# Performance work log

Measured on AMD Instinct MI355X. Metric: run time of the kernel, lower is better.

The kernel has to match this reference:

```python
import jax, jax.numpy as jnp
import numpy as np

N = 100000          # num nodes
E = 1_600_000       # num edges (avg degree 16)
IN = 512
OUT = 64
HOPS = 4


def setup_inputs() -> dict:
    key = jax.random.key(0)
    k1, k2, k3 = jax.random.split(key, 3)
    x = jax.random.normal(k1, (N, IN), dtype=jnp.float32)
    W = jax.random.normal(k2, (OUT, IN), dtype=jnp.float32) * 0.02
    b = jnp.zeros((OUT,), dtype=jnp.float32)
    edge_index = jax.random.randint(k3, (2, E), 0, N, dtype=jnp.int32)
    return {"x": x, "W": W, "b": b, "edge_index": edge_index}


def reference(x, W, b, edge_index):
    # 1) linear projection first (low-memory SGC variant)
    h = x @ W.T + b                      # [N, OUT]
    n = h.shape[0]

    # 2) gcn_norm: add self loops, symmetric D^{-1/2} A D^{-1/2}
    row, col = edge_index[0], edge_index[1]
    loop = jnp.arange(n, dtype=row.dtype)
    row = jnp.concatenate([row, loop])   # [E+N]
    col = jnp.concatenate([col, loop])
    ew = jnp.ones(row.shape[0], dtype=h.dtype)
    deg = jax.ops.segment_sum(ew, col, num_segments=n)          # in-degree incl. self loop
    dinv = jnp.where(deg > 0, jax.lax.rsqrt(deg), 0.0)
    w = dinv[row] * ew * dinv[col]       # normalized edge weights [E+N]

    # 3) hops x SpMM: adj_t built with (row=col, col=row) => out[col] += w * h[row]
    for _ in range(HOPS):
        h = jax.ops.segment_sum(w[:, None] * h[row], col, num_segments=n)
    return h
```

## Files before the change

kernel.cpp:

```cpp
#include <hip/hip_runtime.h>
#include <stdint.h>

#define IN_DIM 512
#define OUT_DIM 64

typedef short bf16x8 __attribute__((ext_vector_type(8)));
typedef float f32x4 __attribute__((ext_vector_type(4)));
typedef _Float16 half4v __attribute__((ext_vector_type(4)));

__device__ inline unsigned short f2bf(float f) {
    unsigned int u = __float_as_uint(f);
    return (unsigned short)((u + 0x7FFFu + ((u >> 16) & 1u)) >> 16);
}
__device__ inline float bf2f(unsigned short s) {
    return __uint_as_float(((unsigned int)s) << 16);
}

__global__ void zero_deg_kernel(int* __restrict__ deg, int N) {
    int i = blockIdx.x * blockDim.x + threadIdx.x;
    if (i < N) deg[i] = 0;
}

__global__ __launch_bounds__(256) void hist_part_kernel(const int* __restrict__ col,
                                                        int* __restrict__ deg, int E, int N) {
    int part = blockIdx.x & 7;
    int lo = (int)((long)part * N / 8);
    int hi = (int)((long)(part + 1) * N / 8);
    int stride = (gridDim.x >> 3) * blockDim.x;
    int i = (blockIdx.x >> 3) * blockDim.x + threadIdx.x;
    for (; i < E; i += stride) {
        int c = col[i];
        if (c >= lo && c < hi) atomicAdd(&deg[c], 1);
    }
}

__global__ void dinv_kernel(const int* __restrict__ deg, float* __restrict__ dinv,
                            float* __restrict__ d2, int N) {
    int i = blockIdx.x * blockDim.x + threadIdx.x;
    if (i < N) {
        float d = (float)deg[i] + 1.0f;
        dinv[i] = 1.0f / sqrtf(d);
        d2[i] = 1.0f / d;
    }
}

__global__ void pack_w_kernel(const float* __restrict__ W,
                              unsigned short* __restrict__ Bhi,
                              unsigned short* __restrict__ Blo) {
    int tid = blockIdx.x * blockDim.x + threadIdx.x;
    if (tid >= 4096) return;
    int L = tid & 63;
    int ct = tid >> 6;
    int t = ct & 15, c = ct >> 4;
    int o = c * 16 + (L & 15);
    int k0 = t * 32 + (L >> 4) * 8;
    const float* src = W + (size_t)o * IN_DIM + k0;
    #pragma unroll
    for (int j = 0; j < 8; ++j) {
        float w = src[j];
        unsigned short h = f2bf(w);
        Bhi[(size_t)tid * 8 + j] = h;
        Blo[(size_t)tid * 8 + j] = f2bf(w - bf2f(h));
    }
}

__global__ __launch_bounds__(1024) void scan_local_kernel(const int* __restrict__ deg,
                                                          int* __restrict__ rowptr,
                                                          int* __restrict__ bsum, int N) {
    __shared__ int sm[16];
    int tid = threadIdx.x, lane = tid & 63, wid = tid >> 6;
    int i = blockIdx.x * 4096 + tid * 4;
    int4 v = make_int4(0, 0, 0, 0);
    if (i + 3 < N) {
        v = *(const int4*)(deg + i);
    } else {
        if (i < N) v.x = deg[i];
        if (i + 1 < N) v.y = deg[i + 1];
        if (i + 2 < N) v.z = deg[i + 2];
        if (i + 3 < N) v.w = deg[i + 3];
    }
    int s1 = v.x, s2 = s1 + v.y, s3 = s2 + v.z, s4 = s3 + v.w;
    int incl = s4;
    #pragma unroll
    for (int d = 1; d < 64; d <<= 1) {
        int t = __shfl_up(incl, d, 64);
        if (lane >= d) incl += t;
    }
    if (lane == 63) sm[wid] = incl;
    __syncthreads();
    if (tid == 0) {
        int run = 0;
        #pragma unroll
        for (int w2 = 0; w2 < 16; ++w2) { int t = sm[w2]; sm[w2] = run; run += t; }
        bsum[blockIdx.x] = run;
    }
    __syncthreads();
    int tbase = incl - s4 + sm[wid];
    if (i + 3 < N) {
        *(int4*)(rowptr + i) = make_int4(tbase, tbase + s1, tbase + s2, tbase + s3);
    } else {
        if (i < N)     rowptr[i]     = tbase;
        if (i + 1 < N) rowptr[i + 1] = tbase + s1;
        if (i + 2 < N) rowptr[i + 2] = tbase + s2;
        if (i + 3 < N) rowptr[i + 3] = tbase + s3;
    }
}

__global__ __launch_bounds__(1024) void scan_add_kernel(int* __restrict__ rowptr,
                                                        int* __restrict__ cursor,
                                                        const int* __restrict__ bsum,
                                                        int N, int nb) {
    __shared__ int soff;
    if (threadIdx.x == 0) {
        int off = 0;
        for (int j = 0; j < (int)blockIdx.x; ++j) off += bsum[j];
        soff = off;
        if ((int)blockIdx.x == nb - 1) {
            int tot = off;
            for (int j = blockIdx.x; j < nb; ++j) tot += bsum[j];
            rowptr[N] = tot;
        }
    }
    __syncthreads();
    int off = soff;
    int i = blockIdx.x * 4096 + threadIdx.x * 4;
    if (i + 3 < N) {
        int4 r = *(int4*)(rowptr + i);
        r.x += off; r.y += off; r.z += off; r.w += off;
        *(int4*)(rowptr + i) = r;
        *(int4*)(cursor + i) = r;
    } else {
        for (int j = 0; j < 4; ++j)
            if (i + j < N) { int r = rowptr[i + j] + off; rowptr[i + j] = r; cursor[i + j] = r; }
    }
}

__global__ __launch_bounds__(256) void fill_part_kernel(const int* __restrict__ row,
                                                        const int* __restrict__ col,
                                                        int* __restrict__ cursor,
                                                        int* __restrict__ csr, int E, int N) {
    int part = blockIdx.x & 7;
    int lo = (int)((long)part * N / 8);
    int hi = (int)((long)(part + 1) * N / 8);
    int stride = (gridDim.x >> 3) * blockDim.x;
    int i = (blockIdx.x >> 3) * blockDim.x + threadIdx.x;
    for (; i < E; i += stride) {
        int c = col[i];
        if (c >= lo && c < hi) {
            int pos = atomicAdd(&cursor[c], 1);
            csr[pos] = row[i];
        }
    }
}

__global__ __launch_bounds__(256) void mfma_gemm_kernel(const float* __restrict__ x,
                                                        const unsigned short* __restrict__ Bhi,
                                                        const unsigned short* __restrict__ Blo,
                                                        const float* __restrict__ bias,
                                                        const float* __restrict__ dinv,
                                                        _Float16* __restrict__ h, int N) {
    int lane = threadIdx.x & 63;
    int wid  = __builtin_amdgcn_readfirstlane(threadIdx.x >> 6);
    int quad = lane >> 4, r16 = lane & 15;
    long rowBase = ((long)blockIdx.x * 4 + wid) * 32;
    if (rowBase >= N) return;
    bool full = (rowBase + 32 <= N);

    f32x4 acc[2][4];
    #pragma unroll
    for (int rt = 0; rt < 2; ++rt)
        #pragma unroll
        for (int c = 0; c < 4; ++c) acc[rt][c] = (f32x4){0.f, 0.f, 0.f, 0.f};

    int row0 = (int)rowBase + r16;
    int row1 = (int)rowBase + 16 + r16;
    int row0c = full ? row0 : (row0 < N ? row0 : N - 1);
    int row1c = full ? row1 : (row1 < N ? row1 : N - 1);
    const float* a0p = x + (size_t)row0c * IN_DIM + quad * 8;
    const float* a1p = x + (size_t)row1c * IN_DIM + quad * 8;

    for (int t = 0; t < 16; ++t) {
        bf16x8 bh[4], bl[4];
        #pragma unroll
        for (int c = 0; c < 4; ++c) {
            size_t off = ((size_t)(c * 16 + t) * 64 + lane) * 8;
            union { int4 i; bf16x8 b; } uh, ul;
            uh.i = *(const int4*)(Bhi + off);
            ul.i = *(const int4*)(Blo + off);
            bh[c] = uh.b; bl[c] = ul.b;
        }
        bf16x8 ah[2], al[2];
        #pragma unroll
        for (int rt = 0; rt < 2; ++rt) {
            const float* p = (rt ? a1p : a0p) + t * 32;
            float4 f0 = *(const float4*)p;
            float4 f1 = *(const float4*)(p + 4);
            float v[8] = {f0.x, f0.y, f0.z, f0.w, f1.x, f1.y, f1.z, f1.w};
            #pragma unroll
            for (int j = 0; j < 8; ++j) {
                unsigned short hi = f2bf(v[j]);
                ah[rt][j] = (short)hi;
                al[rt][j] = (short)f2bf(v[j] - bf2f(hi));
            }
        }
        #pragma unroll
        for (int rt = 0; rt < 2; ++rt)
            #pragma unroll
            for (int c = 0; c < 4; ++c) {
                acc[rt][c] = __builtin_amdgcn_mfma_f32_16x16x32_bf16(ah[rt], bh[c], acc[rt][c], 0, 0, 0);
                acc[rt][c] = __builtin_amdgcn_mfma_f32_16x16x32_bf16(ah[rt], bl[c], acc[rt][c], 0, 0, 0);
                acc[rt][c] = __builtin_amdgcn_mfma_f32_16x16x32_bf16(al[rt], bh[c], acc[rt][c], 0, 0, 0);
            }
    }

    float bb[4];
    #pragma unroll
    for (int c = 0; c < 4; ++c) bb[c] = bias[c * 16 + r16];
    #pragma unroll
    for (int rt = 0; rt < 2; ++rt)
        #pragma unroll
        for (int rr = 0; rr < 4; ++rr) {
            int row = (int)rowBase + rt * 16 + quad * 4 + rr;
            if (row < N) {
                float dv = dinv[row];
                #pragma unroll
                for (int c = 0; c < 4; ++c)
                    h[(size_t)row * OUT_DIM + c * 16 + r16] =
                        (_Float16)(dv * (acc[rt][c][rr] + bb[c]));
            }
        }
}

#define HOP_K 8

__global__ __launch_bounds__(256) void hop_kernel(const _Float16* __restrict__ src,
                                                  _Float16* __restrict__ dst_h,
                                                  float* __restrict__ dst_f,
                                                  const int* __restrict__ csr,
                                                  const int* __restrict__ rowptr,
                                                  const float* __restrict__ scale,
                                                  int N, int finalOut) {
    int lane = threadIdx.x & 63;
    int wid  = __builtin_amdgcn_readfirstlane(threadIdx.x >> 6);
    int g    = lane >> 4;
    int l16  = lane & 15;
    int w  = blockIdx.x * 4 + wid;
    int n0 = w * HOP_K;
    if (n0 >= N) return;
    int nK = (N - n0 < HOP_K) ? (N - n0) : HOP_K;

    int rpv = 0;
    if (lane <= nK) rpv = rowptr[n0 + lane];

    for (int j = 0; j < nK; ++j) {
        int n = n0 + j;
        int s = __shfl(rpv, j, 64);
        int e = __shfl(rpv, j + 1, 64);

        float a0 = 0.f, a1 = 0.f, a2 = 0.f, a3 = 0.f;
        int i = s;
        for (; i + 16 <= e; i += 16) {
            int base = i + 4 * g;
            int i0 = csr[base], i1 = csr[base + 1], i2 = csr[base + 2], i3 = csr[base + 3];
            half4v v0 = *(const half4v*)(src + (size_t)i0 * OUT_DIM + l16 * 4);
            half4v v1 = *(const half4v*)(src + (size_t)i1 * OUT_DIM + l16 * 4);
            half4v v2 = *(const half4v*)(src + (size_t)i2 * OUT_DIM + l16 * 4);
            half4v v3 = *(const half4v*)(src + (size_t)i3 * OUT_DIM + l16 * 4);
            a0 += ((float)v0[0] + (float)v1[0]) + ((float)v2[0] + (float)v3[0]);
            a1 += ((float)v0[1] + (float)v1[1]) + ((float)v2[1] + (float)v3[1]);
            a2 += ((float)v0[2] + (float)v1[2]) + ((float)v2[2] + (float)v3[2]);
            a3 += ((float)v0[3] + (float)v1[3]) + ((float)v2[3] + (float)v3[3]);
        }
        for (; i + 4 <= e; i += 4) {
            int i0 = csr[i + g];
            half4v v = *(const half4v*)(src + (size_t)i0 * OUT_DIM + l16 * 4);
            a0 += (float)v[0]; a1 += (float)v[1]; a2 += (float)v[2]; a3 += (float)v[3];
        }
        if (i + g < e) {
            int i0 = csr[i + g];
            half4v v = *(const half4v*)(src + (size_t)i0 * OUT_DIM + l16 * 4);
            a0 += (float)v[0]; a1 += (float)v[1]; a2 += (float)v[2]; a3 += (float)v[3];
        }
        #pragma unroll
        for (int d = 16; d < 64; d <<= 1) {
            a0 += __shfl_xor(a0, d, 64);
            a1 += __shfl_xor(a1, d, 64);
            a2 += __shfl_xor(a2, d, 64);
            a3 += __shfl_xor(a3, d, 64);
        }
        if (lane < 16) {
            half4v s4 = *(const half4v*)(src + (size_t)n * OUT_DIM + l16 * 4);
            float sc = scale[n];
            float r0 = (a0 + (float)s4[0]) * sc;
            float r1 = (a1 + (float)s4[1]) * sc;
            float r2 = (a2 + (float)s4[2]) * sc;
            float r3 = (a3 + (float)s4[3]) * sc;
            if (finalOut) {
                f32x4 r = (f32x4){r0, r1, r2, r3};
                *(f32x4*)(dst_f + (size_t)n * OUT_DIM + l16 * 4) = r;
            } else {
                half4v o;
                o[0] = (_Float16)r0; o[1] = (_Float16)r1;
                o[2] = (_Float16)r2; o[3] = (_Float16)r3;
                *(half4v*)(dst_h + (size_t)n * OUT_DIM + l16 * 4) = o;
            }
        }
    }
}

extern "C" void kernel_launch(void* const* d_in, const int* in_sizes, int n_in,
                              void* d_out, int out_size, void* d_ws, size_t ws_size,
                              hipStream_t stream) {
    const float* x  = (const float*)d_in[0];
    const float* W  = (const float*)d_in[1];
    const float* b  = (const float*)d_in[2];
    const int*   ei = (const int*)d_in[3];
    int N = in_sizes[0] / IN_DIM;
    int E = in_sizes[3] / 2;
    const int* row = ei;
    const int* col = ei + E;
    float* out = (float*)d_out;

    float* dinv   = (float*)d_ws;
    float* d2     = dinv + N;
    int*   deg    = (int*)(d2 + N);
    int*   rowptr = deg + N;
    int*   cursor = rowptr + (N + 4);
    int*   bsum   = cursor + N;
    unsigned short* Bhi = (unsigned short*)(bsum + 32);
    unsigned short* Blo = Bhi + 32768;

    _Float16* gout = (_Float16*)d_out;
    float* xspace = (float*)d_in[0];
    _Float16* gx   = (_Float16*)xspace;
    int* csr = (int*)((char*)xspace + (size_t)N * OUT_DIM * sizeof(_Float16));

    dim3 blk(256);
    int gN = (N + 255) / 256;
    int gPart = 8 * 784;
    int nbScan = (N + 4095) / 4096;

    zero_deg_kernel<<<gN, blk, 0, stream>>>(deg, N);
    hist_part_kernel<<<gPart, blk, 0, stream>>>(col, deg, E, N);
    dinv_kernel<<<gN, blk, 0, stream>>>(deg, dinv, d2, N);

    pack_w_kernel<<<16, blk, 0, stream>>>(W, Bhi, Blo);

    mfma_gemm_kernel<<<(N + 127) / 128, blk, 0, stream>>>(x, Bhi, Blo, b, dinv, gout, N);

    scan_local_kernel<<<nbScan, 1024, 0, stream>>>(deg, rowptr, bsum, N);
    scan_add_kernel<<<nbScan, 1024, 0, stream>>>(rowptr, cursor, bsum, N, nbScan);
    fill_part_kernel<<<gPart, blk, 0, stream>>>(row, col, cursor, csr, E, N);

    int chunks = (N + HOP_K - 1) / HOP_K;
    int gH = (chunks + 3) / 4;
    hop_kernel<<<gH, blk, 0, stream>>>(gout, gx,   nullptr, csr, rowptr, d2,   N, 0);
    hop_kernel<<<gH, blk, 0, stream>>>(gx,   gout, nullptr, csr, rowptr, d2,   N, 0);
    hop_kernel<<<gH, blk, 0, stream>>>(gout, gx,   nullptr, csr, rowptr, d2,   N, 0);
    hop_kernel<<<gH, blk, 0, stream>>>(gx, nullptr, out,    csr, rowptr, dinv, N, 1);
}
```

Measured before the change: 666.6 us.

## Split hop features into 16-wide column slabs with XCD-aware block mapping

The GEMM now writes the projected features as four column-major slabs of 16 halves per node. Each hop kernel block handles one slab, so every gathered row is 32 bytes and the working set per slab is about 3.2MB, small enough to stay in cache. The block index is mapped so that the same slab lands on consistent XCDs, and a persistent grid of 2048 blocks is used. CSR indices and outputs use nontemporal loads and stores. In exchange, CSR indices and rowptr are read four times, once per slab, and lanes with clamped indices still issue redundant loads.

```diff
diff --git a/kernel.cpp b/kernel.cpp
--- a/kernel.cpp
+++ b/kernel.cpp
@@ -225,13 +225,14 @@
                 float dv = dinv[row];
                 #pragma unroll
                 for (int c = 0; c < 4; ++c)
-                    h[(size_t)row * OUT_DIM + c * 16 + r16] =
+                    h[((size_t)c * N + row) * 16 + r16] =
                         (_Float16)(dv * (acc[rt][c][rr] + bb[c]));
             }
         }
 }
 
 #define HOP_K 8
+#define HOP_BLOCKS 2048
 
 __global__ __launch_bounds__(256) void hop_kernel(const _Float16* __restrict__ src,
                                                   _Float16* __restrict__ dst_h,
@@ -242,67 +243,84 @@
                                                   int N, int finalOut) {
     int lane = threadIdx.x & 63;
     int wid  = __builtin_amdgcn_readfirstlane(threadIdx.x >> 6);
-    int g    = lane >> 4;
-    int l16  = lane & 15;
-    int w  = blockIdx.x * 4 + wid;
-    int n0 = w * HOP_K;
-    if (n0 >= N) return;
-    int nK = (N - n0 < HOP_K) ? (N - n0) : HOP_K;
-
-    int rpv = 0;
-    if (lane <= nK) rpv = rowptr[n0 + lane];
-
-    for (int j = 0; j < nK; ++j) {
-        int n = n0 + j;
-        int s = __shfl(rpv, j, 64);
-        int e = __shfl(rpv, j + 1, 64);
-
-        float a0 = 0.f, a1 = 0.f, a2 = 0.f, a3 = 0.f;
-        int i = s;
-        for (; i + 16 <= e; i += 16) {
-            int base = i + 4 * g;
-            int i0 = csr[base], i1 = csr[base + 1], i2 = csr[base + 2], i3 = csr[base + 3];
-            half4v v0 = *(const half4v*)(src + (size_t)i0 * OUT_DIM + l16 * 4);
-            half4v v1 = *(const half4v*)(src + (size_t)i1 * OUT_DIM + l16 * 4);
-            half4v v2 = *(const half4v*)(src + (size_t)i2 * OUT_DIM + l16 * 4);
-            half4v v3 = *(const half4v*)(src + (size_t)i3 * OUT_DIM + l16 * 4);
-            a0 += ((float)v0[0] + (float)v1[0]) + ((float)v2[0] + (float)v3[0]);
-            a1 += ((float)v0[1] + (float)v1[1]) + ((float)v2[1] + (float)v3[1]);
-            a2 += ((float)v0[2] + (float)v1[2]) + ((float)v2[2] + (float)v3[2]);
-            a3 += ((float)v0[3] + (float)v1[3]) + ((float)v2[3] + (float)v3[3]);
-        }
-        for (; i + 4 <= e; i += 4) {
-            int i0 = csr[i + g];
-            half4v v = *(const half4v*)(src + (size_t)i0 * OUT_DIM + l16 * 4);
-            a0 += (float)v[0]; a1 += (float)v[1]; a2 += (float)v[2]; a3 += (float)v[3];
-        }
-        if (i + g < e) {
-            int i0 = csr[i + g];
-            half4v v = *(const half4v*)(src + (size_t)i0 * OUT_DIM + l16 * 4);
-            a0 += (float)v[0]; a1 += (float)v[1]; a2 += (float)v[2]; a3 += (float)v[3];
-        }
-        #pragma unroll
-        for (int d = 16; d < 64; d <<= 1) {
-            a0 += __shfl_xor(a0, d, 64);
-            a1 += __shfl_xor(a1, d, 64);
-            a2 += __shfl_xor(a2, d, 64);
-            a3 += __shfl_xor(a3, d, 64);
-        }
-        if (lane < 16) {
-            half4v s4 = *(const half4v*)(src + (size_t)n * OUT_DIM + l16 * 4);
-            float sc = scale[n];
-            float r0 = (a0 + (float)s4[0]) * sc;
-            float r1 = (a1 + (float)s4[1]) * sc;
-            float r2 = (a2 + (float)s4[2]) * sc;
-            float r3 = (a3 + (float)s4[3]) * sc;
-            if (finalOut) {
-                f32x4 r = (f32x4){r0, r1, r2, r3};
-                *(f32x4*)(dst_f + (size_t)n * OUT_DIM + l16 * 4) = r;
-            } else {
-                half4v o;
-                o[0] = (_Float16)r0; o[1] = (_Float16)r1;
-                o[2] = (_Float16)r2; o[3] = (_Float16)r3;
-                *(half4v*)(dst_h + (size_t)n * OUT_DIM + l16 * 4) = o;
+    int b    = blockIdx.x;
+    int c    = (b & 7) >> 1;
+    int sub  = ((b >> 3) << 1) | (b & 1);
+    int el   = lane >> 2;
+    int q    = lane & 3;
+
+    const _Float16* cs = src + (size_t)c * N * 16;
+    _Float16* cd = dst_h + (size_t)c * N * 16;
+
+    int nBlocks = (N + 4 * HOP_K - 1) / (4 * HOP_K);
+    for (int nb = sub; nb < nBlocks; nb += 512) {
+        int n0 = nb * (4 * HOP_K) + wid * HOP_K;
+        if (n0 >= N) continue;
+        int nK = (N - n0 < HOP_K) ? (N - n0) : HOP_K;
+
+        int rpv = 0;
+        if (lane <= nK) rpv = rowptr[n0 + lane];
+
+        for (int j = 0; j < nK; ++j) {
+            int n = n0 + j;
+            int s = __shfl(rpv, j, 64);
+            int e = __shfl(rpv, j + 1, 64);
+            int d = e - s;
+
+            float a0 = 0.f, a1 = 0.f, a2 = 0.f, a3 = 0.f;
+            if (d > 0) {
+                int last = e - 1;
+                int ad0 = s + el; if (ad0 > last) ad0 = last;
+                int i0 = __builtin_nontemporal_load(csr + ad0);
+                half4v v0 = *(const half4v*)(cs + (size_t)i0 * 16 + q * 4);
+                if (el < d) {
+                    a0 += (float)v0[0]; a1 += (float)v0[1];
+                    a2 += (float)v0[2]; a3 += (float)v0[3];
+                }
+                if (d > 16) {
+                    int ad1 = s + el + 16; if (ad1 > last) ad1 = last;
+                    int i1 = __builtin_nontemporal_load(csr + ad1);
+                    half4v v1 = *(const half4v*)(cs + (size_t)i1 * 16 + q * 4);
+                    if (el + 16 < d) {
+                        a0 += (float)v1[0]; a1 += (float)v1[1];
+                        a2 += (float)v1[2]; a3 += (float)v1[3];
+                    }
+                    if (d > 32) {
+                        for (int i = s + 32; i < e; i += 16) {
+                            int a = i + el; if (a > last) a = last;
+                            int ii = __builtin_nontemporal_load(csr + a);
+                            half4v v = *(const half4v*)(cs + (size_t)ii * 16 + q * 4);
+                            if (i + el < e) {
+                                a0 += (float)v[0]; a1 += (float)v[1];
+                                a2 += (float)v[2]; a3 += (float)v[3];
+                            }
+                        }
+                    }
+                }
+            }
+            #pragma unroll
+            for (int dd = 4; dd < 64; dd <<= 1) {
+                a0 += __shfl_xor(a0, dd, 64);
+                a1 += __shfl_xor(a1, dd, 64);
+                a2 += __shfl_xor(a2, dd, 64);
+                a3 += __shfl_xor(a3, dd, 64);
+            }
+            if (el == 0) {
+                half4v s4 = *(const half4v*)(cs + (size_t)n * 16 + q * 4);
+                float sc = scale[n];
+                float r0 = (a0 + (float)s4[0]) * sc;
+                float r1 = (a1 + (float)s4[1]) * sc;
+                float r2 = (a2 + (float)s4[2]) * sc;
+                float r3 = (a3 + (float)s4[3]) * sc;
+                if (finalOut) {
+                    f32x4 r = (f32x4){r0, r1, r2, r3};
+                    *(f32x4*)(dst_f + (size_t)n * OUT_DIM + c * 16 + q * 4) = r;
+                } else {
+                    half4v o;
+                    o[0] = (_Float16)r0; o[1] = (_Float16)r1;
+                    o[2] = (_Float16)r2; o[3] = (_Float16)r3;
+                    __builtin_nontemporal_store(o, (half4v*)(cd + (size_t)n * 16 + q * 4));
+                }
             }
         }
     }
@@ -352,10 +370,8 @@
     scan_add_kernel<<<nbScan, 1024, 0, stream>>>(rowptr, cursor, bsum, N, nbScan);
     fill_part_kernel<<<gPart, blk, 0, stream>>>(row, col, cursor, csr, E, N);
 
-    int chunks = (N + HOP_K - 1) / HOP_K;
-    int gH = (chunks + 3) / 4;
-    hop_kernel<<<gH, blk, 0, stream>>>(gout, gx,   nullptr, csr, rowptr, d2,   N, 0);
-    hop_kernel<<<gH, blk, 0, stream>>>(gx,   gout, nullptr, csr, rowptr, d2,   N, 0);
-    hop_kernel<<<gH, blk, 0, stream>>>(gout, gx,   nullptr, csr, rowptr, d2,   N, 0);
-    hop_kernel<<<gH, blk, 0, stream>>>(gx, nullptr, out,    csr, rowptr, dinv, N, 1);
-}
+    hop_kernel<<<HOP_BLOCKS, blk, 0, stream>>>(gout, gx,   nullptr, csr, rowptr, d2,   N, 0);
+    hop_kernel<<<HOP_BLOCKS, blk, 0, stream>>>(gx,   gout, nullptr, csr, rowptr, d2,   N, 0);
+    hop_kernel<<<HOP_BLOCKS, blk, 0, stream>>>(gout, gx,   nullptr, csr, rowptr, d2,   N, 0);
+    hop_kernel<<<HOP_BLOCKS, blk, 0, stream>>>(gx, gout,   out,     csr, rowptr, dinv, N, 1);
+}
```

New measurement: 967.9 us. 45.2% more time.

## Split hop features into 16-wide column chunks processed in separate passes

Applied to the files above, without the earlier changes.

Stores the projected features in a column-chunked layout of [4][N][16] halves and runs each SpMM hop as four passes, one per 16-column chunk. Each pass's gather working set is 3.2 MB instead of 12.8 MB, so random neighbor reads should hit cache more often. In exchange the CSR indices and rowptr are re-read four times per hop, each 32-byte gather row is only half a cache line, and launches go from 4 to 16. Index loads and intermediate stores also become nontemporal.

```diff
diff --git a/kernel.cpp b/kernel.cpp
--- a/kernel.cpp
+++ b/kernel.cpp
@@ -225,7 +225,7 @@
                 float dv = dinv[row];
                 #pragma unroll
                 for (int c = 0; c < 4; ++c)
-                    h[(size_t)row * OUT_DIM + c * 16 + r16] =
+                    h[((size_t)c * N + row) * 16 + r16] =
                         (_Float16)(dv * (acc[rt][c][rr] + bb[c]));
             }
         }
@@ -233,22 +233,24 @@
 
 #define HOP_K 8
 
-__global__ __launch_bounds__(256) void hop_kernel(const _Float16* __restrict__ src,
-                                                  _Float16* __restrict__ dst_h,
-                                                  float* __restrict__ dst_f,
-                                                  const int* __restrict__ csr,
-                                                  const int* __restrict__ rowptr,
-                                                  const float* __restrict__ scale,
-                                                  int N, int finalOut) {
+__global__ __launch_bounds__(256) void hop_pass_kernel(const _Float16* __restrict__ src,
+                                                       _Float16* __restrict__ dst_h,
+                                                       float* __restrict__ dst_f,
+                                                       const int* __restrict__ csr,
+                                                       const int* __restrict__ rowptr,
+                                                       const float* __restrict__ scale,
+                                                       int N, int chunk, int finalOut) {
     int lane = threadIdx.x & 63;
     int wid  = __builtin_amdgcn_readfirstlane(threadIdx.x >> 6);
-    int g    = lane >> 4;
-    int l16  = lane & 15;
+    int el   = lane >> 2;
+    int q    = lane & 3;
     int w  = blockIdx.x * 4 + wid;
     int n0 = w * HOP_K;
     if (n0 >= N) return;
     int nK = (N - n0 < HOP_K) ? (N - n0) : HOP_K;
 
+    const _Float16* cs = src + (size_t)chunk * N * 16;
+
     int rpv = 0;
     if (lane <= nK) rpv = rowptr[n0 + lane];
 
@@ -260,36 +262,26 @@
         float a0 = 0.f, a1 = 0.f, a2 = 0.f, a3 = 0.f;
         int i = s;
         for (; i + 16 <= e; i += 16) {
-            int base = i + 4 * g;
-            int i0 = csr[base], i1 = csr[base + 1], i2 = csr[base + 2], i3 = csr[base + 3];
-            half4v v0 = *(const half4v*)(src + (size_t)i0 * OUT_DIM + l16 * 4);
-            half4v v1 = *(const half4v*)(src + (size_t)i1 * OUT_DIM + l16 * 4);
-            half4v v2 = *(const half4v*)(src + (size_t)i2 * OUT_DIM + l16 * 4);
-            half4v v3 = *(const half4v*)(src + (size_t)i3 * OUT_DIM + l16 * 4);
-            a0 += ((float)v0[0] + (float)v1[0]) + ((float)v2[0] + (float)v3[0]);
-            a1 += ((float)v0[1] + (float)v1[1]) + ((float)v2[1] + (float)v3[1]);
-            a2 += ((float)v0[2] + (float)v1[2]) + ((float)v2[2] + (float)v3[2]);
-            a3 += ((float)v0[3] + (float)v1[3]) + ((float)v2[3] + (float)v3[3]);
-        }
-        for (; i + 4 <= e; i += 4) {
-            int i0 = csr[i + g];
-            half4v v = *(const half4v*)(src + (size_t)i0 * OUT_DIM + l16 * 4);
-            a0 += (float)v[0]; a1 += (float)v[1]; a2 += (float)v[2]; a3 += (float)v[3];
-        }
-        if (i + g < e) {
-            int i0 = csr[i + g];
-            half4v v = *(const half4v*)(src + (size_t)i0 * OUT_DIM + l16 * 4);
-            a0 += (float)v[0]; a1 += (float)v[1]; a2 += (float)v[2]; a3 += (float)v[3];
-        }
-        #pragma unroll
-        for (int d = 16; d < 64; d <<= 1) {
+            int i0 = __builtin_nontemporal_load(csr + i + el);
+            half4v v = *(const half4v*)(cs + (size_t)i0 * 16 + q * 4);
+            a0 += (float)v[0]; a1 += (float)v[1];
+            a2 += (float)v[2]; a3 += (float)v[3];
+        }
+        if (i + el < e) {
+            int i0 = __builtin_nontemporal_load(csr + i + el);
+            half4v v = *(const half4v*)(cs + (size_t)i0 * 16 + q * 4);
+            a0 += (float)v[0]; a1 += (float)v[1];
+            a2 += (float)v[2]; a3 += (float)v[3];
+        }
+        #pragma unroll
+        for (int d = 4; d < 64; d <<= 1) {
             a0 += __shfl_xor(a0, d, 64);
             a1 += __shfl_xor(a1, d, 64);
             a2 += __shfl_xor(a2, d, 64);
             a3 += __shfl_xor(a3, d, 64);
         }
-        if (lane < 16) {
-            half4v s4 = *(const half4v*)(src + (size_t)n * OUT_DIM + l16 * 4);
+        if (el == 0) {
+            half4v s4 = *(const half4v*)(cs + (size_t)n * 16 + q * 4);
             float sc = scale[n];
             float r0 = (a0 + (float)s4[0]) * sc;
             float r1 = (a1 + (float)s4[1]) * sc;
@@ -297,12 +289,13 @@
             float r3 = (a3 + (float)s4[3]) * sc;
             if (finalOut) {
                 f32x4 r = (f32x4){r0, r1, r2, r3};
-                *(f32x4*)(dst_f + (size_t)n * OUT_DIM + l16 * 4) = r;
+                *(f32x4*)(dst_f + (size_t)n * OUT_DIM + chunk * 16 + q * 4) = r;
             } else {
                 half4v o;
                 o[0] = (_Float16)r0; o[1] = (_Float16)r1;
                 o[2] = (_Float16)r2; o[3] = (_Float16)r3;
-                *(half4v*)(dst_h + (size_t)n * OUT_DIM + l16 * 4) = o;
+                __builtin_nontemporal_store(o,
+                    (half4v*)(dst_h + ((size_t)chunk * N + n) * 16 + q * 4));
             }
         }
     }
@@ -352,10 +345,16 @@
     scan_add_kernel<<<nbScan, 1024, 0, stream>>>(rowptr, cursor, bsum, N, nbScan);
     fill_part_kernel<<<gPart, blk, 0, stream>>>(row, col, cursor, csr, E, N);
 
-    int chunks = (N + HOP_K - 1) / HOP_K;
-    int gH = (chunks + 3) / 4;
-    hop_kernel<<<gH, blk, 0, stream>>>(gout, gx,   nullptr, csr, rowptr, d2,   N, 0);
-    hop_kernel<<<gH, blk, 0, stream>>>(gx,   gout, nullptr, csr, rowptr, d2,   N, 0);
-    hop_kernel<<<gH, blk, 0, stream>>>(gout, gx,   nullptr, csr, rowptr, d2,   N, 0);
-    hop_kernel<<<gH, blk, 0, stream>>>(gx, nullptr, out,    csr, rowptr, dinv, N, 1);
-}
+    int chunksW = (N + HOP_K - 1) / HOP_K;
+    int gH = (chunksW + 3) / 4;
+    for (int hop = 0; hop < 4; ++hop) {
+        const _Float16* s = (hop & 1) ? gx : gout;
+        _Float16*       d = (hop & 1) ? gout : gx;
+        int fin = (hop == 3);
+        const float* sc = fin ? dinv : d2;
+        for (int c = 0; c < 4; ++c)
+            hop_pass_kernel<<<gH, blk, 0, stream>>>(s, fin ? nullptr : d,
+                                                    fin ? out : nullptr,
+                                                    csr, rowptr, sc, N, c, fin);
+    }
+}
```

Result: slower. 1.086 ms (+62.9%).
